# Kernel tuning notes

Hardware: AMD Instinct MI355X
Metric: run time of the kernel (lower is better)

Reference implementation:

```python
import jax, jax.numpy as jnp
import numpy as np

L = 6          # number of GNN layers
D = 128        # feature_dim (d_model)
H = 4          # num_heads (hardcoded in AttentionalPropagation)
DH = D // H    # per-head dim
N = 2048       # number of segments/keypoints per frame
B = 1          # batch
NAMES = ["self", "cross"] * (L // 2)
EPS = 1e-5     # InstanceNorm1d eps


def _conv1(W, b, x):
    # Conv1d kernel_size=1: W [out,in], x [b,in,n] -> [b,out,n]
    return jnp.einsum('oi,bin->bon', W, x) + b[None, :, None]


def _inorm(x):
    # InstanceNorm1d (affine=False): normalize over the length axis per (batch, channel)
    m = jnp.mean(x, axis=-1, keepdims=True)
    v = jnp.mean((x - m) ** 2, axis=-1, keepdims=True)
    return (x - m) * jax.lax.rsqrt(v + EPS)


def _attn_block(x, src, p):
    Wq, bq, Wk, bk, Wv, bv, Wm, bm, W1, b1, W2, b2 = p
    b_dim, _, n = x.shape
    # view(b, dim, heads, -1): channel axis split as (DH, H)
    q = _conv1(Wq, bq, x).reshape(b_dim, DH, H, -1)
    k = _conv1(Wk, bk, src).reshape(b_dim, DH, H, -1)
    v = _conv1(Wv, bv, src).reshape(b_dim, DH, H, -1)
    scores = jnp.einsum('bdhn,bdhm->bhnm', q, k) / jnp.sqrt(jnp.asarray(DH, x.dtype))
    prob = jax.nn.softmax(scores, axis=-1)
    msg = jnp.einsum('bhnm,bdhm->bdhn', prob, v).reshape(b_dim, D, -1)
    msg = _conv1(Wm, bm, msg)
    # MLP([2D, 2D, D]): Conv1d -> InstanceNorm1d -> ReLU -> Conv1d
    h = _conv1(W1, b1, jnp.concatenate([x, msg], axis=1))
    h = jax.nn.relu(_inorm(h))
    return _conv1(W2, b2, h)


def setup_inputs() -> dict:
    key = jax.random.key(0)
    ks = jax.random.split(key, 14)
    s = 0.05
    f32 = jnp.float32
    return {
        "desc0": jax.random.normal(ks[0], (B, D, N), f32),
        "desc1": jax.random.normal(ks[1], (B, D, N), f32),
        "Wq": jax.random.normal(ks[2], (L, D, D), f32) * s,
        "bq": jnp.zeros((L, D), f32),
        "Wk": jax.random.normal(ks[3], (L, D, D), f32) * s,
        "bk": jnp.zeros((L, D), f32),
        "Wv": jax.random.normal(ks[4], (L, D, D), f32) * s,
        "bv": jnp.zeros((L, D), f32),
        "Wm": jax.random.normal(ks[5], (L, D, D), f32) * s,
        "bm": jnp.zeros((L, D), f32),
        "W1": jax.random.normal(ks[6], (L, 2 * D, 2 * D), f32) * s,
        "b1": jnp.zeros((L, 2 * D), f32),
        "W2": jax.random.normal(ks[7], (L, D, 2 * D), f32) * s,
        "b2": jnp.zeros((L, D), f32),  # nn.init.constant_(mlp[-1].bias, 0.0)
    }


def reference(desc0, desc1, Wq, bq, Wk, bk, Wv, bv, Wm, bm, W1, b1, W2, b2):
    params = (Wq, bq, Wk, bk, Wv, bv, Wm, bm, W1, b1, W2, b2)
    for l in range(L):
        p = tuple(a[l] for a in params)
        if NAMES[l] == 'cross':
            src0, src1 = desc1, desc0
        else:
            src0, src1 = desc0, desc1
        delta0 = _attn_block(desc0, src0, p)
        delta1 = _attn_block(desc1, src1, p)
        desc0 = desc0 + delta0
        desc1 = desc1 + delta1
    return desc0, desc1
```

## Files before the change

kernel.cpp:

```cpp
#include <hip/hip_runtime.h>

#define NN 2048
#define DDIM 128
#define NHEAD 4
#define DH 32
#define NL 6

typedef __attribute__((ext_vector_type(8))) __bf16 bf16x8;
typedef __attribute__((ext_vector_type(4))) float f32x4;

__device__ __forceinline__ unsigned int f2bf(float x) {
  unsigned int u = __float_as_uint(x);
  u += 0x7fff + ((u >> 16) & 1);
  return u >> 16;
}
__device__ __forceinline__ unsigned int pk2(float a, float b) {
  return f2bf(a) | (f2bf(b) << 16);
}
__device__ __forceinline__ float bf2f(unsigned short u) {
  return __uint_as_float(((unsigned int)u) << 16);
}

__global__ __launch_bounds__(256) void wcast_kernel(
    const float* __restrict__ Wq, const float* __restrict__ Wk,
    const float* __restrict__ Wv, const float* __restrict__ W1,
    const float* __restrict__ W2,
    unsigned short* __restrict__ Wqkv, unsigned short* __restrict__ Wb2,
    unsigned short* __restrict__ Wmix) {
  int idx = (blockIdx.x * 256 + threadIdx.x) * 4;
  if (idx >= 688128) return;
  const float* src; unsigned short* dst; int soff, doff;
  if (idx < 98304)       { src = Wq; soff = idx; dst = Wqkv; doff = idx; }
  else if (idx < 196608) { src = Wk; soff = idx - 98304; dst = Wqkv; doff = idx; }
  else if (idx < 294912) { src = Wv; soff = idx - 196608; dst = Wqkv; doff = idx; }
  else if (idx < 491520) { src = W2; soff = idx - 294912; dst = Wb2; doff = soff; }
  else {
    int f = idx - 491520;
    int l = f >> 15, rem = f & 32767;
    int i = rem >> 7, c = rem & 127;
    src = W1; soff = (l << 16) + (i << 8) + c;
    dst = Wmix; doff = (l << 16) + (i << 8) + c;
  }
  float4 v = *(const float4*)&src[soff];
  uint2 p = { pk2(v.x, v.y), pk2(v.z, v.w) };
  *(uint2*)&dst[doff] = p;
}

__global__ __launch_bounds__(256) void wfuse_kernel(
    const float* __restrict__ W1, const float* __restrict__ Wm,
    unsigned short* __restrict__ Wmix,
    const float* __restrict__ bmv, const float* __restrict__ b1,
    float* __restrict__ b1m) {
  const int l = blockIdx.z;
  const int bj = blockIdx.x * 64;
  const int bi = blockIdx.y * 64;
  __shared__ float Ws[32][65];
  __shared__ float Xs[32][64];
  const int t = threadIdx.x;
  const int ti = (t >> 4) << 2;
  const int tj = (t & 15) << 2;
  float acc[4][4] = {{0.f}};
  for (int k0 = 0; k0 < 128; k0 += 32) {
#pragma unroll
    for (int i = 0; i < 8; ++i) {
      int e = t + i * 256;
      int ii = e >> 5, kk = e & 31;
      Ws[kk][ii] = W1[(size_t)(l << 16) + (bi + ii) * 256 + 128 + k0 + kk];
    }
#pragma unroll
    for (int i = 0; i < 2; ++i) {
      int e = t + i * 256;
      int r = e >> 4, c4 = e & 15;
      *(float4*)&Xs[r][c4 * 4] = *(const float4*)&Wm[(size_t)l * 16384 + (k0 + r) * 128 + bj + c4 * 4];
    }
    __syncthreads();
#pragma unroll
    for (int kk = 0; kk < 32; ++kk) {
      float a[4];
      a[0] = Ws[kk][ti]; a[1] = Ws[kk][ti + 1]; a[2] = Ws[kk][ti + 2]; a[3] = Ws[kk][ti + 3];
      float4 b4 = *(const float4*)&Xs[kk][tj];
      float bb[4] = {b4.x, b4.y, b4.z, b4.w};
#pragma unroll
      for (int i = 0; i < 4; ++i)
#pragma unroll
        for (int j = 0; j < 4; ++j) acc[i][j] += a[i] * bb[j];
    }
    __syncthreads();
  }
#pragma unroll
  for (int i = 0; i < 4; ++i) {
    uint2 p = { pk2(acc[i][0], acc[i][1]), pk2(acc[i][2], acc[i][3]) };
    *(uint2*)&Wmix[(size_t)(l << 16) + (bi + ti + i) * 256 + 128 + bj + tj] = p;
  }
  if (blockIdx.x == 0 && blockIdx.y == 0) {
    float a = b1[l * 256 + t];
    const float* wr = &W1[(size_t)(l << 16) + t * 256 + 128];
    const float* bp = &bmv[l * 128];
    for (int k = 0; k < 128; k += 4)
      a += wr[k] * bp[k] + wr[k + 1] * bp[k + 1] + wr[k + 2] * bp[k + 2] + wr[k + 3] * bp[k + 3];
    b1m[l * 256 + t] = a;
  }
}

__global__ __launch_bounds__(256) void desc_cast_kernel(
    const float* __restrict__ d0, const float* __restrict__ d1,
    unsigned short* __restrict__ t0, unsigned short* __restrict__ t1,
    float* __restrict__ o0, float* __restrict__ o1) {
  const float* D = blockIdx.y ? d1 : d0;
  unsigned short* T = blockIdx.y ? t1 : t0;
  float* O = blockIdx.y ? o1 : o0;
  const int n0 = blockIdx.x * 64;
  const int t = threadIdx.x;
  __shared__ __align__(16) unsigned short L[64 * 136];
#pragma unroll
  for (int i = 0; i < 8; ++i) {
    int idx = t + i * 256;
    int c = idx >> 4, nj = (idx & 15) * 4;
    float4 v = *(const float4*)&D[(size_t)c * NN + n0 + nj];
    *(float4*)&O[(size_t)c * NN + n0 + nj] = v;
    L[(nj + 0) * 136 + c] = (unsigned short)f2bf(v.x);
    L[(nj + 1) * 136 + c] = (unsigned short)f2bf(v.y);
    L[(nj + 2) * 136 + c] = (unsigned short)f2bf(v.z);
    L[(nj + 3) * 136 + c] = (unsigned short)f2bf(v.w);
  }
  __syncthreads();
#pragma unroll
  for (int i = 0; i < 4; ++i) {
    int idx = t + i * 256;
    int n = idx >> 4, cj = (idx & 15) * 8;
    uint4 v = *(const uint4*)&L[n * 136 + cj];
    *(uint4*)&T[(size_t)(n0 + n) * 128 + cj] = v;
  }
}

struct MOp {
  const unsigned short* A;
  const float* bias;
  const unsigned short* B1;
  const unsigned short* B2;
  unsigned short* Cb;
  float* Cf;
  const float* Sp;
  int K, ldb, ldc, mode;
};
struct MOps8 { MOp op[8]; };

__global__ __launch_bounds__(256) void mfma_gemm_kernel(MOps8 P) {
  const MOp g = P.op[blockIdx.z];
  const int t = threadIdx.x;
  const int w = t >> 6, lane = t & 63;
  const int col = lane & 15, Qd = lane >> 4;
  const int bm = blockIdx.y * 64;
  const int bn = blockIdx.x * 128;

  __shared__ __align__(16) unsigned short Ws[64 * 40];
  __shared__ __align__(16) unsigned short Xs[128 * 40];
  __shared__ float meanL[256], rstdL[256];
  __shared__ float swS[4][64], swQ[4][64];

  if (g.mode == 4) {
    float s = g.Sp[t * 2], ss = g.Sp[t * 2 + 1];
    float mean = s * (1.0f / NN);
    float var = fmaxf(ss * (1.0f / NN) - mean * mean, 0.f);
    meanL[t] = mean;
    rstdL[t] = rsqrtf(var + 1e-5f);
  }
  if (g.mode == 0 && g.Cf && blockIdx.x == 0 && blockIdx.y == 0) {
    g.Cf[t] = 0.f;
    g.Cf[t + 256] = 0.f;
  }

  f32x4 acc[4][2];
#pragma unroll
  for (int mt = 0; mt < 4; ++mt)
#pragma unroll
    for (int nt = 0; nt < 2; ++nt) acc[mt][nt] = (f32x4){0.f, 0.f, 0.f, 0.f};

  for (int k0 = 0; k0 < g.K; k0 += 32) {
    __syncthreads();
    {
      int row = t >> 2, ko = (t & 3) * 8;
      *(uint4*)&Ws[row * 40 + ko] =
          *(const uint4*)&g.A[(size_t)(bm + row) * g.K + k0 + ko];
    }
    const unsigned short* Bp = g.B1;
    int kk0 = k0;
    if (g.B2 && k0 >= 128) { Bp = g.B2; kk0 = k0 - 128; }
#pragma unroll
    for (int i = 0; i < 2; ++i) {
      int idx = t + i * 256;
      int row = idx >> 2, ko = (idx & 3) * 8;
      uint4 v = *(const uint4*)&Bp[(size_t)(bn + row) * g.ldb + kk0 + ko];
      if (g.mode == 4) {
        union { uint4 q; unsigned short us[8]; } u;
        u.q = v;
#pragma unroll
        for (int j = 0; j < 8; ++j) {
          int k = k0 + ko + j;
          float x = bf2f(u.us[j]);
          x = fmaxf((x - meanL[k]) * rstdL[k], 0.f);
          u.us[j] = (unsigned short)f2bf(x);
        }
        v = u.q;
      }
      *(uint4*)&Xs[row * 40 + ko] = v;
    }
    __syncthreads();
    bf16x8 af[4], bfr[2];
#pragma unroll
    for (int mt = 0; mt < 4; ++mt)
      af[mt] = *(const bf16x8*)&Ws[(mt * 16 + col) * 40 + Qd * 8];
#pragma unroll
    for (int nt = 0; nt < 2; ++nt)
      bfr[nt] = *(const bf16x8*)&Xs[(w * 32 + nt * 16 + col) * 40 + Qd * 8];
#pragma unroll
    for (int mt = 0; mt < 4; ++mt)
#pragma unroll
      for (int nt = 0; nt < 2; ++nt)
        acc[mt][nt] = __builtin_amdgcn_mfma_f32_16x16x32_bf16(af[mt], bfr[nt], acc[mt][nt], 0, 0, 0);
  }

#pragma unroll
  for (int mt = 0; mt < 4; ++mt) {
    const int c0 = bm + mt * 16 + Qd * 4;
    const float b0 = g.bias[c0], b1 = g.bias[c0 + 1];
    const float b2 = g.bias[c0 + 2], b3 = g.bias[c0 + 3];
    float sA[4] = {0.f, 0.f, 0.f, 0.f}, sQ[4] = {0.f, 0.f, 0.f, 0.f};
#pragma unroll
    for (int nt = 0; nt < 2; ++nt) {
      const int n = bn + w * 32 + nt * 16 + col;
      f32x4 a = acc[mt][nt];
      float v0 = a[0] + b0, v1 = a[1] + b1, v2 = a[2] + b2, v3 = a[3] + b3;
      if (g.mode <= 2) {
        if (g.mode == 0) {
          const float sc = 0.17677669529663687f;
          v0 *= sc; v1 *= sc; v2 *= sc; v3 *= sc;
        }
        const int d = c0 >> 2;
        if (g.mode == 1) {
          g.Cb[((size_t)0 * NN + n) * 32 + d] = (unsigned short)f2bf(v0);
          g.Cb[((size_t)1 * NN + n) * 32 + d] = (unsigned short)f2bf(v1);
          g.Cb[((size_t)2 * NN + n) * 32 + d] = (unsigned short)f2bf(v2);
          g.Cb[((size_t)3 * NN + n) * 32 + d] = (unsigned short)f2bf(v3);
        } else {
          g.Cb[(size_t)(0 * 32 + d) * NN + n] = (unsigned short)f2bf(v0);
          g.Cb[(size_t)(1 * 32 + d) * NN + n] = (unsigned short)f2bf(v1);
          g.Cb[(size_t)(2 * 32 + d) * NN + n] = (unsigned short)f2bf(v2);
          g.Cb[(size_t)(3 * 32 + d) * NN + n] = (unsigned short)f2bf(v3);
        }
      } else if (g.mode == 5) {
        uint2 pv = { pk2(v0, v1), pk2(v2, v3) };
        *(uint2*)&g.Cb[(size_t)n * g.ldc + c0] = pv;
        sA[0] += v0; sA[1] += v1; sA[2] += v2; sA[3] += v3;
        sQ[0] += v0 * v0; sQ[1] += v1 * v1; sQ[2] += v2 * v2; sQ[3] += v3 * v3;
      } else {
        float* dp = g.Cf;
        float o0 = dp[(size_t)(c0 + 0) * NN + n] + v0;
        float o1 = dp[(size_t)(c0 + 1) * NN + n] + v1;
        float o2 = dp[(size_t)(c0 + 2) * NN + n] + v2;
        float o3 = dp[(size_t)(c0 + 3) * NN + n] + v3;
        dp[(size_t)(c0 + 0) * NN + n] = o0;
        dp[(size_t)(c0 + 1) * NN + n] = o1;
        dp[(size_t)(c0 + 2) * NN + n] = o2;
        dp[(size_t)(c0 + 3) * NN + n] = o3;
        uint2 pv = { pk2(o0, o1), pk2(o2, o3) };
        *(uint2*)&g.Cb[(size_t)n * 128 + c0] = pv;
      }
    }
    if (g.mode == 5) {
#pragma unroll
      for (int r = 0; r < 4; ++r) {
#pragma unroll
        for (int off = 1; off < 16; off <<= 1) {
          sA[r] += __shfl_xor(sA[r], off);
          sQ[r] += __shfl_xor(sQ[r], off);
        }
      }
      if (col == 0) {
#pragma unroll
        for (int r = 0; r < 4; ++r) {
          swS[w][mt * 16 + Qd * 4 + r] = sA[r];
          swQ[w][mt * 16 + Qd * 4 + r] = sQ[r];
        }
      }
    }
  }
  if (g.mode == 5) {
    __syncthreads();
    if (t < 64) {
      float a = swS[0][t] + swS[1][t] + swS[2][t] + swS[3][t];
      float b = swQ[0][t] + swQ[1][t] + swQ[2][t] + swQ[3][t];
      atomicAdd(&g.Cf[(bm + t) * 2], a);
      atomicAdd(&g.Cf[(bm + t) * 2 + 1], b);
    }
  }
}

__global__ __launch_bounds__(256) void attn_mfma_kernel(
    const unsigned short* __restrict__ Qb0, const unsigned short* __restrict__ Kt0,
    const unsigned short* __restrict__ Vb0, const unsigned short* __restrict__ Qb1,
    const unsigned short* __restrict__ Kt1, const unsigned short* __restrict__ Vb1,
    unsigned short* __restrict__ mgT0, unsigned short* __restrict__ mgT1, int cross) {
  const int z = blockIdx.y, desc = z >> 2, h = z & 3;
  const int t = threadIdx.x;
  const int wid = t >> 6, lane = t & 63;
  const int col = lane & 15, Qd = lane >> 4;
  const int qsub = wid & 1, half = wid >> 1;
  const int qb = blockIdx.x * 32;
  const int q0 = qb + qsub * 16;

  const unsigned short* Qb = desc ? Qb1 : Qb0;
  const int s = cross ? (1 - desc) : desc;
  const unsigned short* Kt = s ? Kt1 : Kt0;
  const unsigned short* Vb = s ? Vb1 : Vb0;

  __shared__ __align__(16) unsigned short SM[12288];
  unsigned short* KtL = SM + half * 4864;
  unsigned short* VL = SM + half * 4864 + 2560;
  unsigned short* PL = SM + 9728 + wid * 640;

  bf16x8 bq;
  {
    union { unsigned short u[8]; bf16x8 v; } tmp;
#pragma unroll
    for (int j = 0; j < 8; ++j)
      tmp.u[j] = Qb[(size_t)(h * 32 + Qd * 8 + j) * NN + q0 + col];
    bq = tmp.v;
  }

  f32x4 o[2];
  o[0] = (f32x4){0.f, 0.f, 0.f, 0.f};
  o[1] = (f32x4){0.f, 0.f, 0.f, 0.f};
  float m = -1e30f, l = 0.f;

  for (int it = 0; it < 16; ++it) {
    __syncthreads();
    {
      const int key = t >> 2, d8 = (t & 3) * 8;
      *(uint4*)&SM[key * 40 + d8] =
          *(const uint4*)&Kt[((size_t)h * NN + it * 64 + key) * 32 + d8];
      *(uint4*)&SM[4864 + key * 40 + d8] =
          *(const uint4*)&Kt[((size_t)h * NN + 1024 + it * 64 + key) * 32 + d8];
      const int dv = t >> 3, c8 = (t & 7) * 8;
      *(uint4*)&SM[2560 + dv * 72 + c8] =
          *(const uint4*)&Vb[(size_t)(h * 32 + dv) * NN + it * 64 + c8];
      *(uint4*)&SM[7424 + dv * 72 + c8] =
          *(const uint4*)&Vb[(size_t)(h * 32 + dv) * NN + 1024 + it * 64 + c8];
    }
    __syncthreads();
#pragma unroll
    for (int sub = 0; sub < 2; ++sub) {
      bf16x8 aK0 = *(const bf16x8*)&KtL[(sub * 32 + col) * 40 + Qd * 8];
      bf16x8 aK1 = *(const bf16x8*)&KtL[(sub * 32 + 16 + col) * 40 + Qd * 8];
      bf16x8 av0 = *(const bf16x8*)&VL[col * 72 + sub * 32 + Qd * 8];
      bf16x8 av1 = *(const bf16x8*)&VL[(16 + col) * 72 + sub * 32 + Qd * 8];
      f32x4 zacc = {0.f, 0.f, 0.f, 0.f};
      f32x4 s0 = __builtin_amdgcn_mfma_f32_16x16x32_bf16(aK0, bq, zacc, 0, 0, 0);
      f32x4 s1 = __builtin_amdgcn_mfma_f32_16x16x32_bf16(aK1, bq, zacc, 0, 0, 0);
      float cm = fmaxf(fmaxf(fmaxf(s0[0], s0[1]), fmaxf(s0[2], s0[3])),
                       fmaxf(fmaxf(s1[0], s1[1]), fmaxf(s1[2], s1[3])));
      cm = fmaxf(cm, __shfl_xor(cm, 16));
      cm = fmaxf(cm, __shfl_xor(cm, 32));
      const float mn = fmaxf(m, cm);
      const float alpha = __expf(m - mn);
      m = mn;
      float p00 = __expf(s0[0] - mn), p01 = __expf(s0[1] - mn);
      float p02 = __expf(s0[2] - mn), p03 = __expf(s0[3] - mn);
      float p10 = __expf(s1[0] - mn), p11 = __expf(s1[1] - mn);
      float p12 = __expf(s1[2] - mn), p13 = __expf(s1[3] - mn);
      float us = (p00 + p01) + (p02 + p03) + (p10 + p11) + (p12 + p13);
      us += __shfl_xor(us, 16);
      us += __shfl_xor(us, 32);
      l = l * alpha + us;
      uint2 w0 = { pk2(p00, p01), pk2(p02, p03) };
      uint2 w1 = { pk2(p10, p11), pk2(p12, p13) };
      *(uint2*)&PL[col * 40 + Qd * 4] = w0;
      *(uint2*)&PL[col * 40 + 16 + Qd * 4] = w1;
      __threadfence_block();
      bf16x8 pb = *(const bf16x8*)&PL[col * 40 + Qd * 8];
      o[0] = o[0] * alpha;
      o[1] = o[1] * alpha;
      o[0] = __builtin_amdgcn_mfma_f32_16x16x32_bf16(av0, pb, o[0], 0, 0, 0);
      o[1] = __builtin_amdgcn_mfma_f32_16x16x32_bf16(av1, pb, o[1], 0, 0, 0);
      __threadfence_block();
    }
  }

  __syncthreads();
  float* fS = (float*)SM;
#pragma unroll
  for (int h2 = 0; h2 < 2; ++h2) {
    *(float4*)&fS[wid * 512 + col * 32 + h2 * 16 + Qd * 4] =
        make_float4(o[h2][0], o[h2][1], o[h2][2], o[h2][3]);
  }
  if (Qd == 0) {
    fS[2048 + wid * 16 + col] = m;
    fS[2112 + wid * 16 + col] = l;
  }
  __syncthreads();
  {
    const int ql = t & 31, dg = t >> 5;
    const int q16 = ql & 15, qs = ql >> 4;
    const int wA = qs, wB = 2 + qs;
    float m0 = fS[2048 + wA * 16 + q16], m1 = fS[2048 + wB * 16 + q16];
    float l0 = fS[2112 + wA * 16 + q16], l1 = fS[2112 + wB * 16 + q16];
    float M = fmaxf(m0, m1);
    float w0 = __expf(m0 - M), w1 = __expf(m1 - M);
    float inv = 1.0f / (w0 * l0 + w1 * l1);
    unsigned short* T = desc ? mgT1 : mgT0;
    const int q = qb + ql;
#pragma unroll
    for (int r = 0; r < 4; ++r) {
      int d = dg * 4 + r;
      float v = (w0 * fS[wA * 512 + q16 * 32 + d] + w1 * fS[wB * 512 + q16 * 32 + d]) * inv;
      T[(size_t)q * 128 + d * 4 + h] = (unsigned short)f2bf(v);
    }
  }
}

extern "C" void kernel_launch(void* const* d_in, const int* in_sizes, int n_in,
                              void* d_out, int out_size, void* d_ws, size_t ws_size,
                              hipStream_t stream) {
  const float* desc0 = (const float*)d_in[0];
  const float* desc1 = (const float*)d_in[1];
  const float* Wq = (const float*)d_in[2];
  const float* bq = (const float*)d_in[3];
  const float* Wk = (const float*)d_in[4];
  const float* bk = (const float*)d_in[5];
  const float* Wv = (const float*)d_in[6];
  const float* bv = (const float*)d_in[7];
  const float* Wm = (const float*)d_in[8];
  const float* bmv = (const float*)d_in[9];
  const float* W1 = (const float*)d_in[10];
  const float* b1 = (const float*)d_in[11];
  const float* W2 = (const float*)d_in[12];
  const float* b2 = (const float*)d_in[13];

  float* out0 = (float*)d_out;
  float* out1 = out0 + (size_t)DDIM * NN;

  float* fws = (float*)d_ws;
  float* Sg0 = fws;
  float* Sg1 = Sg0 + 512;
  float* b1m = Sg1 + 512;
  unsigned short* uws = (unsigned short*)(b1m + 1536);
  unsigned short* dT0 = uws;
  unsigned short* dT1 = uws + 1 * 262144;
  unsigned short* Qb0 = uws + 2 * 262144;
  unsigned short* Qb1 = uws + 3 * 262144;
  unsigned short* Kt0 = uws + 4 * 262144;
  unsigned short* Kt1 = uws + 5 * 262144;
  unsigned short* Vb0 = uws + 6 * 262144;
  unsigned short* Vb1 = uws + 7 * 262144;
  unsigned short* mgT0 = uws + 8 * 262144;
  unsigned short* mgT1 = uws + 9 * 262144;
  unsigned short* HT0 = uws + 10 * 262144;
  unsigned short* HT1 = HT0 + 524288;
  unsigned short* Wqkv = HT1 + 524288;
  unsigned short* Wb2 = Wqkv + 294912;
  unsigned short* Wmix = Wb2 + 196608;

  wcast_kernel<<<672, 256, 0, stream>>>(Wq, Wk, Wv, W1, W2, Wqkv, Wb2, Wmix);
  wfuse_kernel<<<dim3(2, 4, 6), 256, 0, stream>>>(W1, Wm, Wmix, bmv, b1, b1m);
  desc_cast_kernel<<<dim3(32, 2), 256, 0, stream>>>(desc0, desc1, dT0, dT1, out0, out1);

  for (int l = 0; l < NL; ++l) {
    const int cross = l & 1;
    const unsigned short* wq = Wqkv + l * 16384;
    const unsigned short* wk = Wqkv + 98304 + l * 16384;
    const unsigned short* wv = Wqkv + 196608 + l * 16384;
    const unsigned short* wmx = Wmix + l * 65536;
    const unsigned short* w2 = Wb2 + l * 32768;
    const float* bqp = bq + (size_t)l * 128;
    const float* bkp = bk + (size_t)l * 128;
    const float* bvp = bv + (size_t)l * 128;
    const float* b1p = b1m + (size_t)l * 256;
    const float* b2p = b2 + (size_t)l * 128;

    MOps8 Pq = {};
    Pq.op[0] = {wq, bqp, dT0, nullptr, Qb0, Sg0, nullptr, 128, 128, 0, 0};
    Pq.op[1] = {wq, bqp, dT1, nullptr, Qb1, Sg1, nullptr, 128, 128, 0, 0};
    Pq.op[2] = {wk, bkp, dT0, nullptr, Kt0, nullptr, nullptr, 128, 128, 0, 1};
    Pq.op[3] = {wk, bkp, dT1, nullptr, Kt1, nullptr, nullptr, 128, 128, 0, 1};
    Pq.op[4] = {wv, bvp, dT0, nullptr, Vb0, nullptr, nullptr, 128, 128, 0, 2};
    Pq.op[5] = {wv, bvp, dT1, nullptr, Vb1, nullptr, nullptr, 128, 128, 0, 2};
    mfma_gemm_kernel<<<dim3(16, 2, 6), 256, 0, stream>>>(Pq);

    attn_mfma_kernel<<<dim3(64, 8), 256, 0, stream>>>(
        Qb0, Kt0, Vb0, Qb1, Kt1, Vb1, mgT0, mgT1, cross);

    MOps8 P1 = {};
    P1.op[0] = {wmx, b1p, dT0, mgT0, HT0, Sg0, nullptr, 256, 128, 256, 5};
    P1.op[1] = {wmx, b1p, dT1, mgT1, HT1, Sg1, nullptr, 256, 128, 256, 5};
    mfma_gemm_kernel<<<dim3(16, 4, 2), 256, 0, stream>>>(P1);

    MOps8 P2 = {};
    P2.op[0] = {w2, b2p, HT0, nullptr, dT0, out0, Sg0, 256, 256, 128, 4};
    P2.op[1] = {w2, b2p, HT1, nullptr, dT1, out1, Sg1, 256, 256, 128, 4};
    mfma_gemm_kernel<<<dim3(16, 2, 2), 256, 0, stream>>>(P2);
  }
}
```

Measured before the change: 464.8 us.

## Fuse all layer stages into one persistent cooperative kernel with grid syncs

Replaces the 24 per-layer kernel launches (QKV GEMM, attention, MLP1, MLP2) with a single cooperative persistent kernel of 512 blocks that loops over layers, separated by grid-wide syncs. GEMM tiles shrink from 64x128 to 64x64 so each stage exposes more blocks to fill the grid, and the stats-buffer zeroing moves to a dedicated block. The aim is to remove launch gaps and tail effects between small kernels. In exchange it relies on all 512 blocks being co-resident, and adds grid-barrier cost and smaller tiles with less data reuse.

```diff
diff --git a/kernel.cpp b/kernel.cpp
--- a/kernel.cpp
+++ b/kernel.cpp
@@ -1,4 +1,7 @@
 #include <hip/hip_runtime.h>
+#include <hip/hip_cooperative_groups.h>
+
+namespace cg = cooperative_groups;
 
 #define NN 2048
 #define DDIM 128
@@ -133,65 +136,54 @@
   }
 }
 
-struct MOp {
-  const unsigned short* A;
-  const float* bias;
-  const unsigned short* B1;
-  const unsigned short* B2;
-  unsigned short* Cb;
-  float* Cf;
-  const float* Sp;
-  int K, ldb, ldc, mode;
+struct KArgs {
+  const float *bq, *bk, *bv, *b2;
+  float *out0, *out1, *Sg0, *Sg1, *b1m;
+  unsigned short *dT0, *dT1, *Qb0, *Qb1, *Kt0, *Kt1, *Vb0, *Vb1;
+  unsigned short *mgT0, *mgT1, *HT0, *HT1;
+  const unsigned short *Wqkv, *Wb2, *Wmix;
 };
-struct MOps8 { MOp op[8]; };
-
-__global__ __launch_bounds__(256) void mfma_gemm_kernel(MOps8 P) {
-  const MOp g = P.op[blockIdx.z];
-  const int t = threadIdx.x;
+
+__device__ __forceinline__ void gemm_tile(
+    const unsigned short* __restrict__ Aw, const float* __restrict__ bias,
+    const unsigned short* __restrict__ B1, const unsigned short* __restrict__ B2,
+    unsigned short* __restrict__ Cb, float* __restrict__ Cf,
+    const float* __restrict__ Sp,
+    int K, int ldb, int ldc, int mode, int bm, int bn,
+    unsigned short* SM, int t) {
   const int w = t >> 6, lane = t & 63;
   const int col = lane & 15, Qd = lane >> 4;
-  const int bm = blockIdx.y * 64;
-  const int bn = blockIdx.x * 128;
-
-  __shared__ __align__(16) unsigned short Ws[64 * 40];
-  __shared__ __align__(16) unsigned short Xs[128 * 40];
-  __shared__ float meanL[256], rstdL[256];
-  __shared__ float swS[4][64], swQ[4][64];
-
-  if (g.mode == 4) {
-    float s = g.Sp[t * 2], ss = g.Sp[t * 2 + 1];
+  unsigned short* Ws = SM;
+  unsigned short* Xs = SM + 2560;
+  float* fb = (float*)(SM + 5120);
+  float* meanL = fb;
+  float* rstdL = fb + 256;
+  float* swS = fb + 512;
+  float* swQ = fb + 768;
+
+  if (mode == 4) {
+    float s = Sp[t * 2], ss = Sp[t * 2 + 1];
     float mean = s * (1.0f / NN);
     float var = fmaxf(ss * (1.0f / NN) - mean * mean, 0.f);
     meanL[t] = mean;
     rstdL[t] = rsqrtf(var + 1e-5f);
   }
-  if (g.mode == 0 && g.Cf && blockIdx.x == 0 && blockIdx.y == 0) {
-    g.Cf[t] = 0.f;
-    g.Cf[t + 256] = 0.f;
-  }
-
-  f32x4 acc[4][2];
-#pragma unroll
-  for (int mt = 0; mt < 4; ++mt)
-#pragma unroll
-    for (int nt = 0; nt < 2; ++nt) acc[mt][nt] = (f32x4){0.f, 0.f, 0.f, 0.f};
-
-  for (int k0 = 0; k0 < g.K; k0 += 32) {
+
+  f32x4 acc[4];
+#pragma unroll
+  for (int mt = 0; mt < 4; ++mt) acc[mt] = (f32x4){0.f, 0.f, 0.f, 0.f};
+
+  for (int k0 = 0; k0 < K; k0 += 32) {
     __syncthreads();
     {
       int row = t >> 2, ko = (t & 3) * 8;
       *(uint4*)&Ws[row * 40 + ko] =
-          *(const uint4*)&g.A[(size_t)(bm + row) * g.K + k0 + ko];
-    }
-    const unsigned short* Bp = g.B1;
-    int kk0 = k0;
-    if (g.B2 && k0 >= 128) { Bp = g.B2; kk0 = k0 - 128; }
-#pragma unroll
-    for (int i = 0; i < 2; ++i) {
-      int idx = t + i * 256;
-      int row = idx >> 2, ko = (idx & 3) * 8;
-      uint4 v = *(const uint4*)&Bp[(size_t)(bn + row) * g.ldb + kk0 + ko];
-      if (g.mode == 4) {
+          *(const uint4*)&Aw[(size_t)(bm + row) * K + k0 + ko];
+      const unsigned short* Bp = B1;
+      int kk0 = k0;
+      if (B2 && k0 >= 128) { Bp = B2; kk0 = k0 - 128; }
+      uint4 v = *(const uint4*)&Bp[(size_t)(bn + row) * ldb + kk0 + ko];
+      if (mode == 4) {
         union { uint4 q; unsigned short us[8]; } u;
         u.q = v;
 #pragma unroll
@@ -206,68 +198,44 @@
       *(uint4*)&Xs[row * 40 + ko] = v;
     }
     __syncthreads();
-    bf16x8 af[4], bfr[2];
-#pragma unroll
-    for (int mt = 0; mt < 4; ++mt)
-      af[mt] = *(const bf16x8*)&Ws[(mt * 16 + col) * 40 + Qd * 8];
-#pragma unroll
-    for (int nt = 0; nt < 2; ++nt)
-      bfr[nt] = *(const bf16x8*)&Xs[(w * 32 + nt * 16 + col) * 40 + Qd * 8];
-#pragma unroll
-    for (int mt = 0; mt < 4; ++mt)
-#pragma unroll
-      for (int nt = 0; nt < 2; ++nt)
-        acc[mt][nt] = __builtin_amdgcn_mfma_f32_16x16x32_bf16(af[mt], bfr[nt], acc[mt][nt], 0, 0, 0);
-  }
-
+    bf16x8 bfr = *(const bf16x8*)&Xs[(w * 16 + col) * 40 + Qd * 8];
+#pragma unroll
+    for (int mt = 0; mt < 4; ++mt) {
+      bf16x8 af = *(const bf16x8*)&Ws[(mt * 16 + col) * 40 + Qd * 8];
+      acc[mt] = __builtin_amdgcn_mfma_f32_16x16x32_bf16(af, bfr, acc[mt], 0, 0, 0);
+    }
+  }
+
+  const int n = bn + w * 16 + col;
 #pragma unroll
   for (int mt = 0; mt < 4; ++mt) {
     const int c0 = bm + mt * 16 + Qd * 4;
-    const float b0 = g.bias[c0], b1 = g.bias[c0 + 1];
-    const float b2 = g.bias[c0 + 2], b3 = g.bias[c0 + 3];
-    float sA[4] = {0.f, 0.f, 0.f, 0.f}, sQ[4] = {0.f, 0.f, 0.f, 0.f};
-#pragma unroll
-    for (int nt = 0; nt < 2; ++nt) {
-      const int n = bn + w * 32 + nt * 16 + col;
-      f32x4 a = acc[mt][nt];
-      float v0 = a[0] + b0, v1 = a[1] + b1, v2 = a[2] + b2, v3 = a[3] + b3;
-      if (g.mode <= 2) {
-        if (g.mode == 0) {
-          const float sc = 0.17677669529663687f;
-          v0 *= sc; v1 *= sc; v2 *= sc; v3 *= sc;
-        }
-        const int d = c0 >> 2;
-        if (g.mode == 1) {
-          g.Cb[((size_t)0 * NN + n) * 32 + d] = (unsigned short)f2bf(v0);
-          g.Cb[((size_t)1 * NN + n) * 32 + d] = (unsigned short)f2bf(v1);
-          g.Cb[((size_t)2 * NN + n) * 32 + d] = (unsigned short)f2bf(v2);
-          g.Cb[((size_t)3 * NN + n) * 32 + d] = (unsigned short)f2bf(v3);
-        } else {
-          g.Cb[(size_t)(0 * 32 + d) * NN + n] = (unsigned short)f2bf(v0);
-          g.Cb[(size_t)(1 * 32 + d) * NN + n] = (unsigned short)f2bf(v1);
-          g.Cb[(size_t)(2 * 32 + d) * NN + n] = (unsigned short)f2bf(v2);
-          g.Cb[(size_t)(3 * 32 + d) * NN + n] = (unsigned short)f2bf(v3);
-        }
-      } else if (g.mode == 5) {
-        uint2 pv = { pk2(v0, v1), pk2(v2, v3) };
-        *(uint2*)&g.Cb[(size_t)n * g.ldc + c0] = pv;
-        sA[0] += v0; sA[1] += v1; sA[2] += v2; sA[3] += v3;
-        sQ[0] += v0 * v0; sQ[1] += v1 * v1; sQ[2] += v2 * v2; sQ[3] += v3 * v3;
+    const float b0 = bias[c0], b1v = bias[c0 + 1];
+    const float b2v = bias[c0 + 2], b3v = bias[c0 + 3];
+    f32x4 a = acc[mt];
+    float v0 = a[0] + b0, v1 = a[1] + b1v, v2 = a[2] + b2v, v3 = a[3] + b3v;
+    if (mode <= 2) {
+      if (mode == 0) {
+        const float sc = 0.17677669529663687f;
+        v0 *= sc; v1 *= sc; v2 *= sc; v3 *= sc;
+      }
+      const int d = c0 >> 2;
+      if (mode == 1) {
+        Cb[((size_t)0 * NN + n) * 32 + d] = (unsigned short)f2bf(v0);
+        Cb[((size_t)1 * NN + n) * 32 + d] = (unsigned short)f2bf(v1);
+        Cb[((size_t)2 * NN + n) * 32 + d] = (unsigned short)f2bf(v2);
+        Cb[((size_t)3 * NN + n) * 32 + d] = (unsigned short)f2bf(v3);
       } else {
-        float* dp = g.Cf;
-        float o0 = dp[(size_t)(c0 + 0) * NN + n] + v0;
-        float o1 = dp[(size_t)(c0 + 1) * NN + n] + v1;
-        float o2 = dp[(size_t)(c0 + 2) * NN + n] + v2;
-        float o3 = dp[(size_t)(c0 + 3) * NN + n] + v3;
-        dp[(size_t)(c0 + 0) * NN + n] = o0;
-        dp[(size_t)(c0 + 1) * NN + n] = o1;
-        dp[(size_t)(c0 + 2) * NN + n] = o2;
-        dp[(size_t)(c0 + 3) * NN + n] = o3;
-        uint2 pv = { pk2(o0, o1), pk2(o2, o3) };
-        *(uint2*)&g.Cb[(size_t)n * 128 + c0] = pv;
+        Cb[(size_t)(0 * 32 + d) * NN + n] = (unsigned short)f2bf(v0);
+        Cb[(size_t)(1 * 32 + d) * NN + n] = (unsigned short)f2bf(v1);
+        Cb[(size_t)(2 * 32 + d) * NN + n] = (unsigned short)f2bf(v2);
+        Cb[(size_t)(3 * 32 + d) * NN + n] = (unsigned short)f2bf(v3);
       }
-    }
-    if (g.mode == 5) {
+    } else if (mode == 5) {
+      uint2 pv = { pk2(v0, v1), pk2(v2, v3) };
+      *(uint2*)&Cb[(size_t)n * ldc + c0] = pv;
+      float sA[4] = {v0, v1, v2, v3};
+      float sQ[4] = {v0 * v0, v1 * v1, v2 * v2, v3 * v3};
 #pragma unroll
       for (int r = 0; r < 4; ++r) {
 #pragma unroll
@@ -279,42 +247,50 @@
       if (col == 0) {
 #pragma unroll
         for (int r = 0; r < 4; ++r) {
-          swS[w][mt * 16 + Qd * 4 + r] = sA[r];
-          swQ[w][mt * 16 + Qd * 4 + r] = sQ[r];
+          swS[w * 64 + mt * 16 + Qd * 4 + r] = sA[r];
+          swQ[w * 64 + mt * 16 + Qd * 4 + r] = sQ[r];
         }
       }
-    }
-  }
-  if (g.mode == 5) {
+    } else {
+      float o0 = Cf[(size_t)(c0 + 0) * NN + n] + v0;
+      float o1 = Cf[(size_t)(c0 + 1) * NN + n] + v1;
+      float o2 = Cf[(size_t)(c0 + 2) * NN + n] + v2;
+      float o3 = Cf[(size_t)(c0 + 3) * NN + n] + v3;
+      Cf[(size_t)(c0 + 0) * NN + n] = o0;
+      Cf[(size_t)(c0 + 1) * NN + n] = o1;
+      Cf[(size_t)(c0 + 2) * NN + n] = o2;
+      Cf[(size_t)(c0 + 3) * NN + n] = o3;
+      uint2 pv = { pk2(o0, o1), pk2(o2, o3) };
+      *(uint2*)&Cb[(size_t)n * ldc + c0] = pv;
+    }
+  }
+  if (mode == 5) {
     __syncthreads();
     if (t < 64) {
-      float a = swS[0][t] + swS[1][t] + swS[2][t] + swS[3][t];
-      float b = swQ[0][t] + swQ[1][t] + swQ[2][t] + swQ[3][t];
-      atomicAdd(&g.Cf[(bm + t) * 2], a);
-      atomicAdd(&g.Cf[(bm + t) * 2 + 1], b);
-    }
-  }
-}
-
-__global__ __launch_bounds__(256) void attn_mfma_kernel(
-    const unsigned short* __restrict__ Qb0, const unsigned short* __restrict__ Kt0,
-    const unsigned short* __restrict__ Vb0, const unsigned short* __restrict__ Qb1,
-    const unsigned short* __restrict__ Kt1, const unsigned short* __restrict__ Vb1,
-    unsigned short* __restrict__ mgT0, unsigned short* __restrict__ mgT1, int cross) {
-  const int z = blockIdx.y, desc = z >> 2, h = z & 3;
-  const int t = threadIdx.x;
+      float a = swS[t] + swS[64 + t] + swS[128 + t] + swS[192 + t];
+      float b = swQ[t] + swQ[64 + t] + swQ[128 + t] + swQ[192 + t];
+      atomicAdd(&Cf[(bm + t) * 2], a);
+      atomicAdd(&Cf[(bm + t) * 2 + 1], b);
+    }
+  }
+}
+
+__device__ __forceinline__ void attn_job(const KArgs& A, int l, int job,
+                                         unsigned short* SM, int t) {
+  const int z = job >> 6;
+  const int desc = z >> 2, h = z & 3;
+  const int cross = l & 1;
   const int wid = t >> 6, lane = t & 63;
   const int col = lane & 15, Qd = lane >> 4;
   const int qsub = wid & 1, half = wid >> 1;
-  const int qb = blockIdx.x * 32;
+  const int qb = (job & 63) * 32;
   const int q0 = qb + qsub * 16;
 
-  const unsigned short* Qb = desc ? Qb1 : Qb0;
+  const unsigned short* Qb = desc ? A.Qb1 : A.Qb0;
   const int s = cross ? (1 - desc) : desc;
-  const unsigned short* Kt = s ? Kt1 : Kt0;
-  const unsigned short* Vb = s ? Vb1 : Vb0;
-
-  __shared__ __align__(16) unsigned short SM[12288];
+  const unsigned short* Kt = s ? A.Kt1 : A.Kt0;
+  const unsigned short* Vb = s ? A.Vb1 : A.Vb0;
+
   unsigned short* KtL = SM + half * 4864;
   unsigned short* VL = SM + half * 4864 + 2560;
   unsigned short* PL = SM + 9728 + wid * 640;
@@ -331,7 +307,7 @@
   f32x4 o[2];
   o[0] = (f32x4){0.f, 0.f, 0.f, 0.f};
   o[1] = (f32x4){0.f, 0.f, 0.f, 0.f};
-  float m = -1e30f, l = 0.f;
+  float m = -1e30f, l2 = 0.f;
 
   for (int it = 0; it < 16; ++it) {
     __syncthreads();
@@ -371,7 +347,7 @@
       float us = (p00 + p01) + (p02 + p03) + (p10 + p11) + (p12 + p13);
       us += __shfl_xor(us, 16);
       us += __shfl_xor(us, 32);
-      l = l * alpha + us;
+      l2 = l2 * alpha + us;
       uint2 w0 = { pk2(p00, p01), pk2(p02, p03) };
       uint2 w1 = { pk2(p10, p11), pk2(p12, p13) };
       *(uint2*)&PL[col * 40 + Qd * 4] = w0;
@@ -395,7 +371,7 @@
   }
   if (Qd == 0) {
     fS[2048 + wid * 16 + col] = m;
-    fS[2112 + wid * 16 + col] = l;
+    fS[2112 + wid * 16 + col] = l2;
   }
   __syncthreads();
   {
@@ -407,7 +383,7 @@
     float M = fmaxf(m0, m1);
     float w0 = __expf(m0 - M), w1 = __expf(m1 - M);
     float inv = 1.0f / (w0 * l0 + w1 * l1);
-    unsigned short* T = desc ? mgT1 : mgT0;
+    unsigned short* T = desc ? A.mgT1 : A.mgT0;
     const int q = qb + ql;
 #pragma unroll
     for (int r = 0; r < 4; ++r) {
@@ -415,6 +391,55 @@
       float v = (w0 * fS[wA * 512 + q16 * 32 + d] + w1 * fS[wB * 512 + q16 * 32 + d]) * inv;
       T[(size_t)q * 128 + d * 4 + h] = (unsigned short)f2bf(v);
     }
+  }
+}
+
+__global__ __launch_bounds__(256, 2) void fused_layers_kernel(KArgs A) {
+  cg::grid_group grid = cg::this_grid();
+  __shared__ __align__(16) unsigned short SM[12288];
+  const int t = threadIdx.x;
+  const int bid = blockIdx.x;
+  const int G = gridDim.x;
+
+  for (int l = 0; l < NL; ++l) {
+    for (int j = bid; j < 384; j += G) {
+      const int opk = j >> 6, rem = j & 63;
+      const int bn = (rem >> 1) * 64, bm = (rem & 1) * 64;
+      const int dsc = opk & 1, kind = opk >> 1;
+      const unsigned short* wA = A.Wqkv + kind * 98304 + l * 16384;
+      const float* bias = (kind == 0 ? A.bq : kind == 1 ? A.bk : A.bv) + l * 128;
+      const unsigned short* B1 = dsc ? A.dT1 : A.dT0;
+      unsigned short* Cb = (kind == 0) ? (dsc ? A.Qb1 : A.Qb0)
+                         : (kind == 1) ? (dsc ? A.Kt1 : A.Kt0)
+                                       : (dsc ? A.Vb1 : A.Vb0);
+      gemm_tile(wA, bias, B1, nullptr, Cb, nullptr, nullptr,
+                128, 128, 0, kind, bm, bn, SM, t);
+    }
+    if (bid == 448) {
+      A.Sg0[t] = 0.f; A.Sg0[t + 256] = 0.f;
+      A.Sg1[t] = 0.f; A.Sg1[t + 256] = 0.f;
+    }
+    grid.sync();
+    attn_job(A, l, bid, SM, t);
+    grid.sync();
+    for (int j = bid; j < 256; j += G) {
+      const int dsc = j & 1, rem = j >> 1;
+      const int bn = (rem & 31) * 64, bm = (rem >> 5) * 64;
+      gemm_tile(A.Wmix + l * 65536, A.b1m + l * 256,
+                dsc ? A.dT1 : A.dT0, dsc ? A.mgT1 : A.mgT0,
+                dsc ? A.HT1 : A.HT0, dsc ? A.Sg1 : A.Sg0, nullptr,
+                256, 128, 256, 5, bm, bn, SM, t);
+    }
+    grid.sync();
+    for (int j = bid; j < 128; j += G) {
+      const int dsc = j & 1, rem = j >> 1;
+      const int bn = (rem & 31) * 64, bm = (rem >> 5) * 64;
+      gemm_tile(A.Wb2 + l * 32768, A.b2 + l * 128,
+                dsc ? A.HT1 : A.HT0, nullptr,
+                dsc ? A.dT1 : A.dT0, dsc ? A.out1 : A.out0, dsc ? A.Sg1 : A.Sg0,
+                256, 256, 128, 4, bm, bn, SM, t);
+    }
+    grid.sync();
   }
 }
 
@@ -464,39 +489,14 @@
   wfuse_kernel<<<dim3(2, 4, 6), 256, 0, stream>>>(W1, Wm, Wmix, bmv, b1, b1m);
   desc_cast_kernel<<<dim3(32, 2), 256, 0, stream>>>(desc0, desc1, dT0, dT1, out0, out1);
 
-  for (int l = 0; l < NL; ++l) {
-    const int cross = l & 1;
-    const unsigned short* wq = Wqkv + l * 16384;
-    const unsigned short* wk = Wqkv + 98304 + l * 16384;
-    const unsigned short* wv = Wqkv + 196608 + l * 16384;
-    const unsigned short* wmx = Wmix + l * 65536;
-    const unsigned short* w2 = Wb2 + l * 32768;
-    const float* bqp = bq + (size_t)l * 128;
-    const float* bkp = bk + (size_t)l * 128;
-    const float* bvp = bv + (size_t)l * 128;
-    const float* b1p = b1m + (size_t)l * 256;
-    const float* b2p = b2 + (size_t)l * 128;
-
-    MOps8 Pq = {};
-    Pq.op[0] = {wq, bqp, dT0, nullptr, Qb0, Sg0, nullptr, 128, 128, 0, 0};
-    Pq.op[1] = {wq, bqp, dT1, nullptr, Qb1, Sg1, nullptr, 128, 128, 0, 0};
-    Pq.op[2] = {wk, bkp, dT0, nullptr, Kt0, nullptr, nullptr, 128, 128, 0, 1};
-    Pq.op[3] = {wk, bkp, dT1, nullptr, Kt1, nullptr, nullptr, 128, 128, 0, 1};
-    Pq.op[4] = {wv, bvp, dT0, nullptr, Vb0, nullptr, nullptr, 128, 128, 0, 2};
-    Pq.op[5] = {wv, bvp, dT1, nullptr, Vb1, nullptr, nullptr, 128, 128, 0, 2};
-    mfma_gemm_kernel<<<dim3(16, 2, 6), 256, 0, stream>>>(Pq);
-
-    attn_mfma_kernel<<<dim3(64, 8), 256, 0, stream>>>(
-        Qb0, Kt0, Vb0, Qb1, Kt1, Vb1, mgT0, mgT1, cross);
-
-    MOps8 P1 = {};
-    P1.op[0] = {wmx, b1p, dT0, mgT0, HT0, Sg0, nullptr, 256, 128, 256, 5};
-    P1.op[1] = {wmx, b1p, dT1, mgT1, HT1, Sg1, nullptr, 256, 128, 256, 5};
-    mfma_gemm_kernel<<<dim3(16, 4, 2), 256, 0, stream>>>(P1);
-
-    MOps8 P2 = {};
-    P2.op[0] = {w2, b2p, HT0, nullptr, dT0, out0, Sg0, 256, 256, 128, 4};
-    P2.op[1] = {w2, b2p, HT1, nullptr, dT1, out1, Sg1, 256, 256, 128, 4};
-    mfma_gemm_kernel<<<dim3(16, 2, 2), 256, 0, stream>>>(P2);
-  }
-}
+  KArgs ka;
+  ka.bq = bq; ka.bk = bk; ka.bv = bv; ka.b2 = b2;
+  ka.out0 = out0; ka.out1 = out1; ka.Sg0 = Sg0; ka.Sg1 = Sg1; ka.b1m = b1m;
+  ka.dT0 = dT0; ka.dT1 = dT1; ka.Qb0 = Qb0; ka.Qb1 = Qb1;
+  ka.Kt0 = Kt0; ka.Kt1 = Kt1; ka.Vb0 = Vb0; ka.Vb1 = Vb1;
+  ka.mgT0 = mgT0; ka.mgT1 = mgT1; ka.HT0 = HT0; ka.HT1 = HT1;
+  ka.Wqkv = Wqkv; ka.Wb2 = Wb2; ka.Wmix = Wmix;
+  void* params[] = { (void*)&ka };
+  (void)hipLaunchCooperativeKernel((const void*)fused_layers_kernel,
+                                   dim3(512), dim3(256), params, 0, stream);
+}
```

New measurement: 1.821 ms. +291.7%, slower.

## Split attention keys across four independent waves with per-wave LDS and no block barriers

Applied to the files above, without the earlier changes.

The attention kernel now gives each block 16 queries and has each of its four waves own a quarter of the keys. Each wave stages its own K/V tiles in private LDS, which removes the two block-wide barriers per iteration and the thread fences. The four partial softmax states are merged at the end. The query scale now folds in log2(e) so exp2f can replace __expf, and the grid doubles to 128x8 with a launch_bounds occupancy hint. In exchange, each wave loads K/V for itself without cooperative reuse, and nothing overlaps the global loads with compute.

```diff
diff --git a/kernel.cpp b/kernel.cpp
--- a/kernel.cpp
+++ b/kernel.cpp
@@ -233,7 +233,7 @@
       float v0 = a[0] + b0, v1 = a[1] + b1, v2 = a[2] + b2, v3 = a[3] + b3;
       if (g.mode <= 2) {
         if (g.mode == 0) {
-          const float sc = 0.17677669529663687f;
+          const float sc = 0.25503488f;
           v0 *= sc; v1 *= sc; v2 *= sc; v3 *= sc;
         }
         const int d = c0 >> 2;
@@ -296,7 +296,7 @@
   }
 }
 
-__global__ __launch_bounds__(256) void attn_mfma_kernel(
+__global__ __launch_bounds__(256, 4) void attn_mfma_kernel(
     const unsigned short* __restrict__ Qb0, const unsigned short* __restrict__ Kt0,
     const unsigned short* __restrict__ Vb0, const unsigned short* __restrict__ Qb1,
     const unsigned short* __restrict__ Kt1, const unsigned short* __restrict__ Vb1,
@@ -305,114 +305,103 @@
   const int t = threadIdx.x;
   const int wid = t >> 6, lane = t & 63;
   const int col = lane & 15, Qd = lane >> 4;
-  const int qsub = wid & 1, half = wid >> 1;
-  const int qb = blockIdx.x * 32;
-  const int q0 = qb + qsub * 16;
+  const int qb = blockIdx.x * 16;
 
   const unsigned short* Qb = desc ? Qb1 : Qb0;
   const int s = cross ? (1 - desc) : desc;
   const unsigned short* Kt = s ? Kt1 : Kt0;
   const unsigned short* Vb = s ? Vb1 : Vb0;
 
-  __shared__ __align__(16) unsigned short SM[12288];
-  unsigned short* KtL = SM + half * 4864;
-  unsigned short* VL = SM + half * 4864 + 2560;
-  unsigned short* PL = SM + 9728 + wid * 640;
+  __shared__ __align__(16) unsigned short SM[12800];
+  unsigned short* KtW = SM + wid * 3200;
+  unsigned short* VW = SM + wid * 3200 + 1280;
+  unsigned short* PW = SM + wid * 3200 + 2560;
 
   bf16x8 bq;
   {
     union { unsigned short u[8]; bf16x8 v; } tmp;
 #pragma unroll
     for (int j = 0; j < 8; ++j)
-      tmp.u[j] = Qb[(size_t)(h * 32 + Qd * 8 + j) * NN + q0 + col];
+      tmp.u[j] = Qb[(size_t)(h * 32 + Qd * 8 + j) * NN + qb + col];
     bq = tmp.v;
   }
 
-  f32x4 o[2];
-  o[0] = (f32x4){0.f, 0.f, 0.f, 0.f};
-  o[1] = (f32x4){0.f, 0.f, 0.f, 0.f};
+  f32x4 o0 = {0.f, 0.f, 0.f, 0.f}, o1 = {0.f, 0.f, 0.f, 0.f};
   float m = -1e30f, l = 0.f;
 
+  const int kq = wid * 512;
   for (int it = 0; it < 16; ++it) {
-    __syncthreads();
-    {
-      const int key = t >> 2, d8 = (t & 3) * 8;
-      *(uint4*)&SM[key * 40 + d8] =
-          *(const uint4*)&Kt[((size_t)h * NN + it * 64 + key) * 32 + d8];
-      *(uint4*)&SM[4864 + key * 40 + d8] =
-          *(const uint4*)&Kt[((size_t)h * NN + 1024 + it * 64 + key) * 32 + d8];
-      const int dv = t >> 3, c8 = (t & 7) * 8;
-      *(uint4*)&SM[2560 + dv * 72 + c8] =
-          *(const uint4*)&Vb[(size_t)(h * 32 + dv) * NN + it * 64 + c8];
-      *(uint4*)&SM[7424 + dv * 72 + c8] =
-          *(const uint4*)&Vb[(size_t)(h * 32 + dv) * NN + 1024 + it * 64 + c8];
-    }
-    __syncthreads();
-#pragma unroll
-    for (int sub = 0; sub < 2; ++sub) {
-      bf16x8 aK0 = *(const bf16x8*)&KtL[(sub * 32 + col) * 40 + Qd * 8];
-      bf16x8 aK1 = *(const bf16x8*)&KtL[(sub * 32 + 16 + col) * 40 + Qd * 8];
-      bf16x8 av0 = *(const bf16x8*)&VL[col * 72 + sub * 32 + Qd * 8];
-      bf16x8 av1 = *(const bf16x8*)&VL[(16 + col) * 72 + sub * 32 + Qd * 8];
-      f32x4 zacc = {0.f, 0.f, 0.f, 0.f};
-      f32x4 s0 = __builtin_amdgcn_mfma_f32_16x16x32_bf16(aK0, bq, zacc, 0, 0, 0);
-      f32x4 s1 = __builtin_amdgcn_mfma_f32_16x16x32_bf16(aK1, bq, zacc, 0, 0, 0);
-      float cm = fmaxf(fmaxf(fmaxf(s0[0], s0[1]), fmaxf(s0[2], s0[3])),
-                       fmaxf(fmaxf(s1[0], s1[1]), fmaxf(s1[2], s1[3])));
-      cm = fmaxf(cm, __shfl_xor(cm, 16));
-      cm = fmaxf(cm, __shfl_xor(cm, 32));
-      const float mn = fmaxf(m, cm);
-      const float alpha = __expf(m - mn);
-      m = mn;
-      float p00 = __expf(s0[0] - mn), p01 = __expf(s0[1] - mn);
-      float p02 = __expf(s0[2] - mn), p03 = __expf(s0[3] - mn);
-      float p10 = __expf(s1[0] - mn), p11 = __expf(s1[1] - mn);
-      float p12 = __expf(s1[2] - mn), p13 = __expf(s1[3] - mn);
-      float us = (p00 + p01) + (p02 + p03) + (p10 + p11) + (p12 + p13);
-      us += __shfl_xor(us, 16);
-      us += __shfl_xor(us, 32);
-      l = l * alpha + us;
-      uint2 w0 = { pk2(p00, p01), pk2(p02, p03) };
-      uint2 w1 = { pk2(p10, p11), pk2(p12, p13) };
-      *(uint2*)&PL[col * 40 + Qd * 4] = w0;
-      *(uint2*)&PL[col * 40 + 16 + Qd * 4] = w1;
-      __threadfence_block();
-      bf16x8 pb = *(const bf16x8*)&PL[col * 40 + Qd * 8];
-      o[0] = o[0] * alpha;
-      o[1] = o[1] * alpha;
-      o[0] = __builtin_amdgcn_mfma_f32_16x16x32_bf16(av0, pb, o[0], 0, 0, 0);
-      o[1] = __builtin_amdgcn_mfma_f32_16x16x32_bf16(av1, pb, o[1], 0, 0, 0);
-      __threadfence_block();
-    }
+    const int k0 = kq + it * 32;
+#pragma unroll
+    for (int jj = 0; jj < 2; ++jj) {
+      int e = lane + jj * 64;
+      int r4 = e >> 2, seg = (e & 3) * 8;
+      *(uint4*)&KtW[r4 * 40 + seg] =
+          *(const uint4*)&Kt[((size_t)h * NN + k0 + r4) * 32 + seg];
+      *(uint4*)&VW[r4 * 40 + seg] =
+          *(const uint4*)&Vb[(size_t)(h * 32 + r4) * NN + k0 + seg];
+    }
+    bf16x8 aK0 = *(const bf16x8*)&KtW[col * 40 + Qd * 8];
+    bf16x8 aK1 = *(const bf16x8*)&KtW[(16 + col) * 40 + Qd * 8];
+    bf16x8 av0 = *(const bf16x8*)&VW[col * 40 + Qd * 8];
+    bf16x8 av1 = *(const bf16x8*)&VW[(16 + col) * 40 + Qd * 8];
+    f32x4 z4 = {0.f, 0.f, 0.f, 0.f};
+    f32x4 s0 = __builtin_amdgcn_mfma_f32_16x16x32_bf16(aK0, bq, z4, 0, 0, 0);
+    f32x4 s1 = __builtin_amdgcn_mfma_f32_16x16x32_bf16(aK1, bq, z4, 0, 0, 0);
+    float cm = fmaxf(fmaxf(fmaxf(s0[0], s0[1]), fmaxf(s0[2], s0[3])),
+                     fmaxf(fmaxf(s1[0], s1[1]), fmaxf(s1[2], s1[3])));
+    cm = fmaxf(cm, __shfl_xor(cm, 16));
+    cm = fmaxf(cm, __shfl_xor(cm, 32));
+    const float mn = fmaxf(m, cm);
+    const float alpha = exp2f(m - mn);
+    m = mn;
+    float p00 = exp2f(s0[0] - mn), p01 = exp2f(s0[1] - mn);
+    float p02 = exp2f(s0[2] - mn), p03 = exp2f(s0[3] - mn);
+    float p10 = exp2f(s1[0] - mn), p11 = exp2f(s1[1] - mn);
+    float p12 = exp2f(s1[2] - mn), p13 = exp2f(s1[3] - mn);
+    float us = (p00 + p01) + (p02 + p03) + (p10 + p11) + (p12 + p13);
+    us += __shfl_xor(us, 16);
+    us += __shfl_xor(us, 32);
+    l = l * alpha + us;
+    uint2 w0 = { pk2(p00, p01), pk2(p02, p03) };
+    uint2 w1 = { pk2(p10, p11), pk2(p12, p13) };
+    *(uint2*)&PW[col * 40 + Qd * 4] = w0;
+    *(uint2*)&PW[col * 40 + 16 + Qd * 4] = w1;
+    bf16x8 pb = *(const bf16x8*)&PW[col * 40 + Qd * 8];
+    o0 = o0 * alpha;
+    o1 = o1 * alpha;
+    o0 = __builtin_amdgcn_mfma_f32_16x16x32_bf16(av0, pb, o0, 0, 0, 0);
+    o1 = __builtin_amdgcn_mfma_f32_16x16x32_bf16(av1, pb, o1, 0, 0, 0);
   }
 
   __syncthreads();
   float* fS = (float*)SM;
-#pragma unroll
-  for (int h2 = 0; h2 < 2; ++h2) {
-    *(float4*)&fS[wid * 512 + col * 32 + h2 * 16 + Qd * 4] =
-        make_float4(o[h2][0], o[h2][1], o[h2][2], o[h2][3]);
-  }
+  *(float4*)&fS[wid * 576 + col * 36 + Qd * 4] =
+      make_float4(o0[0], o0[1], o0[2], o0[3]);
+  *(float4*)&fS[wid * 576 + col * 36 + 16 + Qd * 4] =
+      make_float4(o1[0], o1[1], o1[2], o1[3]);
   if (Qd == 0) {
-    fS[2048 + wid * 16 + col] = m;
-    fS[2112 + wid * 16 + col] = l;
+    fS[2304 + wid * 16 + col] = m;
+    fS[2368 + wid * 16 + col] = l;
   }
   __syncthreads();
   {
-    const int ql = t & 31, dg = t >> 5;
-    const int q16 = ql & 15, qs = ql >> 4;
-    const int wA = qs, wB = 2 + qs;
-    float m0 = fS[2048 + wA * 16 + q16], m1 = fS[2048 + wB * 16 + q16];
-    float l0 = fS[2112 + wA * 16 + q16], l1 = fS[2112 + wB * 16 + q16];
-    float M = fmaxf(m0, m1);
-    float w0 = __expf(m0 - M), w1 = __expf(m1 - M);
-    float inv = 1.0f / (w0 * l0 + w1 * l1);
+    const int q16 = t >> 4, dg = t & 15;
+    float m0 = fS[2304 + q16], m1 = fS[2304 + 16 + q16];
+    float m2 = fS[2304 + 32 + q16], m3 = fS[2304 + 48 + q16];
+    float M = fmaxf(fmaxf(m0, m1), fmaxf(m2, m3));
+    float w0 = exp2f(m0 - M), w1 = exp2f(m1 - M);
+    float w2 = exp2f(m2 - M), w3 = exp2f(m3 - M);
+    float L = w0 * fS[2368 + q16] + w1 * fS[2368 + 16 + q16] +
+              w2 * fS[2368 + 32 + q16] + w3 * fS[2368 + 48 + q16];
+    float inv = 1.0f / L;
     unsigned short* T = desc ? mgT1 : mgT0;
-    const int q = qb + ql;
-#pragma unroll
-    for (int r = 0; r < 4; ++r) {
-      int d = dg * 4 + r;
-      float v = (w0 * fS[wA * 512 + q16 * 32 + d] + w1 * fS[wB * 512 + q16 * 32 + d]) * inv;
+    const int q = qb + q16;
+#pragma unroll
+    for (int r = 0; r < 2; ++r) {
+      int d = dg * 2 + r;
+      float v = (w0 * fS[0 * 576 + q16 * 36 + d] + w1 * fS[1 * 576 + q16 * 36 + d] +
+                 w2 * fS[2 * 576 + q16 * 36 + d] + w3 * fS[3 * 576 + q16 * 36 + d]) * inv;
       T[(size_t)q * 128 + d * 4 + h] = (unsigned short)f2bf(v);
     }
   }
@@ -486,7 +475,7 @@
     Pq.op[5] = {wv, bvp, dT1, nullptr, Vb1, nullptr, nullptr, 128, 128, 0, 2};
     mfma_gemm_kernel<<<dim3(16, 2, 6), 256, 0, stream>>>(Pq);
 
-    attn_mfma_kernel<<<dim3(64, 8), 256, 0, stream>>>(
+    attn_mfma_kernel<<<dim3(128, 8), 256, 0, stream>>>(
         Qb0, Kt0, Vb0, Qb1, Kt1, Vb1, mgT0, mgT1, cross);
 
     MOps8 P1 = {};
```

Result: faster. 447.4 us (-3.8%).
